# Kernel tuning notes

Measured on AMD Instinct MI355X. Metric: run time of the kernel, lower is better.

## Reference

```python
import jax, jax.numpy as jnp
import numpy as np

N_QUBITS = 10
Q_DEPTH = 6
MAX_LAYERS = 15
DIM = 2 ** N_QUBITS
INV_SQRT2 = 0.7071067811865476

# PennyLane ordering: wire 0 is the most-significant bit of the state index.
# All gates (H, RY, CNOT) are real, so the state stays real float32.

def _split(state, wire):
    a = 2 ** wire
    b = 2 ** (N_QUBITS - wire - 1)
    return state.reshape(-1, a, 2, b)

def apply_h(state, wire):
    s = _split(state, wire)
    s0, s1 = s[:, :, 0], s[:, :, 1]
    out = jnp.stack([(s0 + s1) * INV_SQRT2, (s0 - s1) * INV_SQRT2], axis=2)
    return out.reshape(-1, DIM)

def apply_ry(state, theta, wire):
    # theta: scalar (shared weight) or (B,) per-sample angle
    c = jnp.cos(theta * 0.5).reshape(-1, 1, 1)
    sn = jnp.sin(theta * 0.5).reshape(-1, 1, 1)
    s = _split(state, wire)
    s0, s1 = s[:, :, 0], s[:, :, 1]
    out = jnp.stack([c * s0 - sn * s1, sn * s0 + c * s1], axis=2)
    return out.reshape(-1, DIM)

def apply_cnot(state, ctrl):
    # CNOT on adjacent wires [ctrl, ctrl+1]
    a = 2 ** ctrl
    b = 2 ** (N_QUBITS - ctrl - 2)
    s = state.reshape(-1, a, 2, 2, b)
    out = jnp.stack([s[:, :, 0], s[:, :, 1, ::-1]], axis=2)
    return out.reshape(-1, DIM)

def expval_z(state):
    # <Z_j> = P(qubit j = 0) - P(qubit j = 1)
    zs = []
    for w in range(N_QUBITS):
        s = _split(state, w)
        p = s * s
        zs.append(jnp.sum(p[:, :, 0], axis=(1, 2)) - jnp.sum(p[:, :, 1], axis=(1, 2)))
    return jnp.stack(zs, axis=1)  # (B, n_qubits)

def simulate(q_in, q_params):
    B = q_in.shape[0]
    qw = q_params.reshape(MAX_LAYERS, N_QUBITS)
    state = jnp.zeros((B, DIM), q_in.dtype).at[:, 0].set(1.0)
    for w in range(N_QUBITS):
        state = apply_h(state, w)
    for w in range(N_QUBITS):
        state = apply_ry(state, q_in[:, w], w)
    for k in range(Q_DEPTH):
        for i in range(0, N_QUBITS - 1, 2):
            state = apply_cnot(state, i)
        for i in range(1, N_QUBITS - 1, 2):
            state = apply_cnot(state, i)
        for w in range(N_QUBITS):
            state = apply_ry(state, qw[k + 1, w], w)
    return expval_z(state)

def setup_inputs() -> dict:
    key = jax.random.key(0)
    k1, k2, k3, k4, k5 = jax.random.split(key, 5)
    B, D_IN, N_CLASSES = 8192, 512, 2
    return {
        "input_features": jax.random.normal(k1, (B, D_IN), jnp.float32),
        "W_red": jax.random.normal(k2, (N_QUBITS, D_IN), jnp.float32) * 0.04,
        "b_red": jnp.zeros((N_QUBITS,), jnp.float32),
        "q_params": 0.01 * jax.random.normal(k3, (MAX_LAYERS * N_QUBITS,), jnp.float32),
        "W_post": jax.random.normal(k4, (N_CLASSES, N_QUBITS), jnp.float32) * 0.3,
        "b_post": jax.random.normal(k5, (N_CLASSES,), jnp.float32) * 0.01,
    }

def reference(input_features, W_red, b_red, q_params, W_post, b_post):
    pre_out = input_features @ W_red.T + b_red           # (B, n_qubits)
    q_in = jnp.tanh(pre_out) * (np.pi / 2.0)             # angles in (-pi/2, pi/2)
    q_out = simulate(q_in, q_params)                     # (B, n_qubits) PauliZ expvals
    return q_out @ W_post.T + b_post                     # (B, n_classes)
```

## Files before the change

### kernel.cpp

```cpp
#include <hip/hip_runtime.h>
#include <math.h>

#define QDEPTH 6


__device__ __forceinline__ float shx(float v, int m) { return __shfl_xor(v, m, 64); }

template<int CTRL>
__device__ __forceinline__ float dpp_mov(float v) {
  int i = __float_as_int(v);
  int r = __builtin_amdgcn_update_dpp(i, i, CTRL, 0xF, 0xF, true);
  return __int_as_float(r);
}

template<int CTRL>
__device__ __forceinline__ float dpp_add0(float v) {
  int i = __float_as_int(v);
  int r = __builtin_amdgcn_update_dpp(0, i, CTRL, 0xF, 0xF, false);
  return v + __int_as_float(r);
}

__device__ __forceinline__ float wave_sum(float v) {
  v = dpp_add0<0x111>(v);
  v = dpp_add0<0x112>(v);
  v = dpp_add0<0x114>(v);
  v = dpp_add0<0x118>(v);
  v = dpp_add0<0x142>(v);
  v = dpp_add0<0x143>(v);
  return v;
}

__device__ __forceinline__ float bcast63(float v) {
  return __int_as_float(__builtin_amdgcn_readlane(__float_as_int(v), 63));
}

__device__ __forceinline__ void pl32_swap(float& a, float& b) {
  asm("v_permlane32_swap_b32 %0, %1" : "+v"(a), "+v"(b));
}
__device__ __forceinline__ void pl16_swap(float& a, float& b) {
  asm("v_permlane16_swap_b32 %0, %1" : "+v"(a), "+v"(b));
}

template<bool IS32>
__device__ __forceinline__ void ry_pl(float (&x)[16], float c, float s) {
#pragma unroll
  for (int r = 0; r < 16; r += 2) {
    float a = x[r], b = x[r + 1];
    if (IS32) pl32_swap(a, b); else pl16_swap(a, b);
    float n0 = c * a - s * b;
    float n1 = s * a + c * b;
    if (IS32) pl32_swap(n0, n1); else pl16_swap(n0, n1);
    x[r] = n0; x[r + 1] = n1;
  }
}

template<int CTRL>
__device__ __forceinline__ void ry_dpp(float (&x)[16], float c, float sg) {
#pragma unroll
  for (int r = 0; r < 16; ++r) {
    float p = dpp_mov<CTRL>(x[r]);
    x[r] = c * x[r] + sg * p;
  }
}

template<int M>
__device__ __forceinline__ void ry_sh(float (&x)[16], float c, float sg) {
#pragma unroll
  for (int r = 0; r < 16; ++r) {
    float p = shx(x[r], M);
    x[r] = c * x[r] + sg * p;
  }
}

template<int JM>
__device__ __forceinline__ void ry_reg(float (&x)[16], float c, float s) {
#pragma unroll
  for (int r = 0; r < 16; ++r)
    if (!(r & JM)) {
      float x0 = x[r], x1 = x[r | JM];
      x[r]      = c * x0 - s * x1;
      x[r | JM] = s * x0 + c * x1;
    }
}

template<int MC, int MT>
__device__ __forceinline__ void cnot_rr(float (&x)[16]) {
#pragma unroll
  for (int r = 0; r < 16; ++r)
    if ((r & MC) && !(r & MT)) {
      float t = x[r]; x[r] = x[r | MT]; x[r | MT] = t;
    }
}

__device__ __forceinline__ void cnot_lr56(float (&x)[16], int lane) {
  bool cb = lane & 1;
#pragma unroll
  for (int r = 0; r < 8; ++r) {
    float lo = x[r], hi = x[r + 8];
    x[r]     = cb ? hi : lo;
    x[r + 8] = cb ? lo : hi;
  }
}

__global__ void __launch_bounds__(256) qnet_kernel(
    const float* __restrict__ inp,
    const float* __restrict__ Wred,
    const float* __restrict__ bred,
    const float* __restrict__ qp,
    const float* __restrict__ Wpost,
    const float* __restrict__ bpost,
    float* __restrict__ out,
    int B) {
  int tid  = blockIdx.x * 256 + threadIdx.x;
  int wv   = tid >> 6;
  int lane = tid & 63;
  if (wv >= B) return;

  int o = lane ^ (((lane >> 4) & 1) << 3) ^ (((lane >> 2) & 1) << 1);
  int psrc = o ^ (((o >> 5) & 1) << 4) ^ (((o >> 3) & 1) << 2) ^ ((o >> 1) & 1);

  const float4* row4 = (const float4*)(inp + (size_t)wv * 512);
  float4 a0 = row4[lane], a1 = row4[lane + 64];
  float th[10];
#pragma unroll
  for (int q = 0; q < 10; ++q) {
    const float4* w4 = (const float4*)(Wred + q * 512);
    float4 b0 = w4[lane], b1 = w4[lane + 64];
    float t = a0.x * b0.x + a0.y * b0.y + a0.z * b0.z + a0.w * b0.w;
    t += a1.x * b1.x + a1.y * b1.y + a1.z * b1.z + a1.w * b1.w;
    th[q] = t;
  }

  float g0[10], g1[10];
#pragma unroll
  for (int q = 0; q < 10; ++q) {
    float tot = bcast63(wave_sum(th[q])) + bred[q];
    float xc = fminf(fmaxf(tot, -15.f), 15.f);
    float u = __expf(2.f * xc);
    float tanhv = (u - 1.f) * __builtin_amdgcn_rcpf(u + 1.f);
    float t = tanhv * 0.78539816339744831f;
    float c = __cosf(t), s = __sinf(t);
    g0[q] = (c - s) * 0.70710678118654752f;
    g1[q] = (c + s) * 0.70710678118654752f;
  }
  float lf = 1.f;
#pragma unroll
  for (int w = 0; w < 6; ++w)
    lf *= ((lane >> (5 - w)) & 1) ? g1[w] : g0[w];
  float f67[4], f89[4];
#pragma unroll
  for (int i = 0; i < 4; ++i) {
    f67[i] = ((i & 2) ? g1[6] : g0[6]) * ((i & 1) ? g1[7] : g0[7]);
    f89[i] = ((i & 2) ? g1[8] : g0[8]) * ((i & 1) ? g1[9] : g0[9]);
  }
  float x[16];
#pragma unroll
  for (int r = 0; r < 16; ++r) x[r] = lf * f67[r >> 2] * f89[r & 3];

#pragma unroll
  for (int k = 0; k < QDEPTH; ++k) {
    const float* qr = qp + (k + 1) * 10;
#pragma unroll
    for (int r = 0; r < 16; ++r) x[r] = __shfl(x[r], psrc, 64);
    cnot_rr<8, 4>(x);
    cnot_rr<2, 1>(x);
    cnot_lr56(x, lane);
    cnot_rr<4, 2>(x);

    float t, c, s, sg;
    t = qr[0] * 0.5f; c = __cosf(t); s = __sinf(t); ry_pl<true>(x, c, s);
    t = qr[1] * 0.5f; c = __cosf(t); s = __sinf(t); ry_pl<false>(x, c, s);
    t = qr[2] * 0.5f; c = __cosf(t); s = __sinf(t);
    sg = (lane & 8) ? s : -s; ry_sh<8>(x, c, sg);
    t = qr[3] * 0.5f; c = __cosf(t); s = __sinf(t);
    sg = (lane & 4) ? s : -s; ry_sh<4>(x, c, sg);
    t = qr[4] * 0.5f; c = __cosf(t); s = __sinf(t);
    sg = (lane & 2) ? s : -s; ry_dpp<0x4E>(x, c, sg);
    t = qr[5] * 0.5f; c = __cosf(t); s = __sinf(t);
    sg = (lane & 1) ? s : -s; ry_dpp<0xB1>(x, c, sg);
    t = qr[6] * 0.5f; c = __cosf(t); s = __sinf(t); ry_reg<8>(x, c, s);
    t = qr[7] * 0.5f; c = __cosf(t); s = __sinf(t); ry_reg<4>(x, c, s);
    t = qr[8] * 0.5f; c = __cosf(t); s = __sinf(t); ry_reg<2>(x, c, s);
    t = qr[9] * 0.5f; c = __cosf(t); s = __sinf(t); ry_reg<1>(x, c, s);
  }

  float S = 0.f, z6 = 0.f, z7 = 0.f, z8 = 0.f, z9 = 0.f;
#pragma unroll
  for (int r = 0; r < 16; ++r) {
    float q2 = x[r] * x[r];
    S  += q2;
    z6 += (r & 8) ? -q2 : q2;
    z7 += (r & 4) ? -q2 : q2;
    z8 += (r & 2) ? -q2 : q2;
    z9 += (r & 1) ? -q2 : q2;
  }
  float A0 = 0.f, A1 = 0.f;
#pragma unroll
  for (int w = 0; w < 6; ++w) {
    bool b = (lane >> (5 - w)) & 1;
    A0 += b ? -Wpost[w] : Wpost[w];
    A1 += b ? -Wpost[10 + w] : Wpost[10 + w];
  }
  float o0 = A0 * S + Wpost[6] * z6 + Wpost[7] * z7 + Wpost[8] * z8 + Wpost[9] * z9;
  float o1 = A1 * S + Wpost[16] * z6 + Wpost[17] * z7 + Wpost[18] * z8 + Wpost[19] * z9;
  o0 = wave_sum(o0);
  o1 = wave_sum(o1);
  if (lane == 63) {
    out[2 * (size_t)wv]     = o0 + bpost[0];
    out[2 * (size_t)wv + 1] = o1 + bpost[1];
  }
}

extern "C" void kernel_launch(void* const* d_in, const int* in_sizes, int n_in,
                              void* d_out, int out_size, void* d_ws, size_t ws_size,
                              hipStream_t stream) {
  const float* inp   = (const float*)d_in[0];
  const float* Wred  = (const float*)d_in[1];
  const float* bred  = (const float*)d_in[2];
  const float* qp    = (const float*)d_in[3];
  const float* Wpost = (const float*)d_in[4];
  const float* bpost = (const float*)d_in[5];
  float* out = (float*)d_out;

  int B = in_sizes[0] / 512;
  int threads = 256;
  int blocks = (B * 64 + threads - 1) / threads;
  qnet_kernel<<<blocks, threads, 0, stream>>>(inp, Wred, bred, qp, Wpost, bpost, out, B);
}
```

Measured before the change: 113.3 us.

## Pack state amplitudes into float2 pairs and use packed FP32 math

Reorganizes the 16 per-lane amplitudes into 8 float2 pairs and applies the RY gates with v_pk_fma/v_pk_mul packed FP32 instructions, halving the VALU instruction count for the rotation arithmetic. The CNOT permutations and the in-register RY gates are reordered and remapped so that the lane-bit CNOT becomes a per-lane coefficient selection inside the qubit-6 rotation, and the qubit-9 pair rotation is folded into the swap pattern. Inline asm for the packed ops may block compiler scheduling and fusion, and the shuffles and DPP moves still run per scalar, so the gains depend on how much of the time is arithmetic versus cross-lane movement.

New measurement: 109.8 us. 1.03x faster.

```diff
diff --git a/kernel.cpp b/kernel.cpp
--- a/kernel.cpp
+++ b/kernel.cpp
@@ -2,6 +2,8 @@
 #include <math.h>
 
 #define QDEPTH 6
+
+typedef float f2 __attribute__((ext_vector_type(2)));
 
 
 __device__ __forceinline__ float shx(float v, int m) { return __shfl_xor(v, m, 64); }
@@ -41,65 +43,11 @@
   asm("v_permlane16_swap_b32 %0, %1" : "+v"(a), "+v"(b));
 }
 
-template<bool IS32>
-__device__ __forceinline__ void ry_pl(float (&x)[16], float c, float s) {
-#pragma unroll
-  for (int r = 0; r < 16; r += 2) {
-    float a = x[r], b = x[r + 1];
-    if (IS32) pl32_swap(a, b); else pl16_swap(a, b);
-    float n0 = c * a - s * b;
-    float n1 = s * a + c * b;
-    if (IS32) pl32_swap(n0, n1); else pl16_swap(n0, n1);
-    x[r] = n0; x[r + 1] = n1;
-  }
-}
-
-template<int CTRL>
-__device__ __forceinline__ void ry_dpp(float (&x)[16], float c, float sg) {
-#pragma unroll
-  for (int r = 0; r < 16; ++r) {
-    float p = dpp_mov<CTRL>(x[r]);
-    x[r] = c * x[r] + sg * p;
-  }
-}
-
-template<int M>
-__device__ __forceinline__ void ry_sh(float (&x)[16], float c, float sg) {
-#pragma unroll
-  for (int r = 0; r < 16; ++r) {
-    float p = shx(x[r], M);
-    x[r] = c * x[r] + sg * p;
-  }
-}
-
-template<int JM>
-__device__ __forceinline__ void ry_reg(float (&x)[16], float c, float s) {
-#pragma unroll
-  for (int r = 0; r < 16; ++r)
-    if (!(r & JM)) {
-      float x0 = x[r], x1 = x[r | JM];
-      x[r]      = c * x0 - s * x1;
-      x[r | JM] = s * x0 + c * x1;
-    }
-}
-
-template<int MC, int MT>
-__device__ __forceinline__ void cnot_rr(float (&x)[16]) {
-#pragma unroll
-  for (int r = 0; r < 16; ++r)
-    if ((r & MC) && !(r & MT)) {
-      float t = x[r]; x[r] = x[r | MT]; x[r | MT] = t;
-    }
-}
-
-__device__ __forceinline__ void cnot_lr56(float (&x)[16], int lane) {
-  bool cb = lane & 1;
-#pragma unroll
-  for (int r = 0; r < 8; ++r) {
-    float lo = x[r], hi = x[r + 8];
-    x[r]     = cb ? hi : lo;
-    x[r + 8] = cb ? lo : hi;
-  }
+__device__ __forceinline__ f2 pk_mul(f2 a, f2 b) {
+  f2 d; asm("v_pk_mul_f32 %0, %1, %2" : "=v"(d) : "v"(a), "v"(b)); return d;
+}
+__device__ __forceinline__ f2 pk_fma(f2 a, f2 b, f2 c) {
+  f2 d; asm("v_pk_fma_f32 %0, %1, %2, %3" : "=v"(d) : "v"(a), "v"(b), "v"(c)); return d;
 }
 
 __global__ void __launch_bounds__(256) qnet_kernel(
@@ -147,53 +95,158 @@
 #pragma unroll
   for (int w = 0; w < 6; ++w)
     lf *= ((lane >> (5 - w)) & 1) ? g1[w] : g0[w];
-  float f67[4], f89[4];
-#pragma unroll
-  for (int i = 0; i < 4; ++i) {
-    f67[i] = ((i & 2) ? g1[6] : g0[6]) * ((i & 1) ? g1[7] : g0[7]);
-    f89[i] = ((i & 2) ? g1[8] : g0[8]) * ((i & 1) ? g1[9] : g0[9]);
-  }
-  float x[16];
-#pragma unroll
-  for (int r = 0; r < 16; ++r) x[r] = lf * f67[r >> 2] * f89[r & 3];
+  float f67v[4];
+#pragma unroll
+  for (int j = 0; j < 4; ++j)
+    f67v[j] = ((j & 2) ? g1[6] : g0[6]) * ((j & 1) ? g1[7] : g0[7]);
+  f2 F89v[2];
+  F89v[0] = (f2){ g0[8] * g0[9], g0[8] * g1[9] };
+  F89v[1] = (f2){ g1[8] * g0[9], g1[8] * g1[9] };
+  f2 x2[8];
+#pragma unroll
+  for (int i = 0; i < 8; ++i) {
+    float m = lf * f67v[i >> 1];
+    x2[i] = (f2){ m * F89v[i & 1].x, m * F89v[i & 1].y };
+  }
+
+  bool cb = lane & 1;
 
 #pragma unroll
   for (int k = 0; k < QDEPTH; ++k) {
     const float* qr = qp + (k + 1) * 10;
-#pragma unroll
-    for (int r = 0; r < 16; ++r) x[r] = __shfl(x[r], psrc, 64);
-    cnot_rr<8, 4>(x);
-    cnot_rr<2, 1>(x);
-    cnot_lr56(x, lane);
-    cnot_rr<4, 2>(x);
-
-    float t, c, s, sg;
-    t = qr[0] * 0.5f; c = __cosf(t); s = __sinf(t); ry_pl<true>(x, c, s);
-    t = qr[1] * 0.5f; c = __cosf(t); s = __sinf(t); ry_pl<false>(x, c, s);
-    t = qr[2] * 0.5f; c = __cosf(t); s = __sinf(t);
-    sg = (lane & 8) ? s : -s; ry_sh<8>(x, c, sg);
-    t = qr[3] * 0.5f; c = __cosf(t); s = __sinf(t);
-    sg = (lane & 4) ? s : -s; ry_sh<4>(x, c, sg);
-    t = qr[4] * 0.5f; c = __cosf(t); s = __sinf(t);
-    sg = (lane & 2) ? s : -s; ry_dpp<0x4E>(x, c, sg);
-    t = qr[5] * 0.5f; c = __cosf(t); s = __sinf(t);
-    sg = (lane & 1) ? s : -s; ry_dpp<0xB1>(x, c, sg);
-    t = qr[6] * 0.5f; c = __cosf(t); s = __sinf(t); ry_reg<8>(x, c, s);
-    t = qr[7] * 0.5f; c = __cosf(t); s = __sinf(t); ry_reg<4>(x, c, s);
-    t = qr[8] * 0.5f; c = __cosf(t); s = __sinf(t); ry_reg<2>(x, c, s);
-    t = qr[9] * 0.5f; c = __cosf(t); s = __sinf(t); ry_reg<1>(x, c, s);
-  }
-
-  float S = 0.f, z6 = 0.f, z7 = 0.f, z8 = 0.f, z9 = 0.f;
-#pragma unroll
-  for (int r = 0; r < 16; ++r) {
-    float q2 = x[r] * x[r];
-    S  += q2;
-    z6 += (r & 8) ? -q2 : q2;
-    z7 += (r & 4) ? -q2 : q2;
-    z8 += (r & 2) ? -q2 : q2;
-    z9 += (r & 1) ? -q2 : q2;
-  }
+
+#pragma unroll
+    for (int i = 0; i < 8; ++i) {
+      float lo = __shfl(x2[i].x, psrc, 64);
+      float hi = __shfl(x2[i].y, psrc, 64);
+      x2[i] = (f2){lo, hi};
+    }
+    { f2 t = x2[4]; x2[4] = x2[6]; x2[6] = t;
+      t = x2[5]; x2[5] = x2[7]; x2[7] = t; }
+    { f2 t = x2[2]; x2[2] = x2[3]; x2[3] = t;
+      t = x2[6]; x2[6] = x2[7]; x2[7] = t; }
+
+    { float t9 = qr[9] * 0.5f; float c = __cosf(t9), s = __sinf(t9);
+#pragma unroll
+      for (int i = 0; i < 8; ++i) {
+        bool flg = (i == 1 || i == 2 || i == 5 || i == 6);
+        float lo = x2[i].x, hi = x2[i].y;
+        float nlo, nhi;
+        if (flg) { nlo = c * hi - s * lo; nhi = s * hi + c * lo; }
+        else     { nlo = c * lo - s * hi; nhi = s * lo + c * hi; }
+        x2[i] = (f2){nlo, nhi};
+      } }
+
+    { float t6 = qr[6] * 0.5f; float c = __cosf(t6), s = __sinf(t6);
+      float Ac = cb ? -s : c;  float Bc = cb ? c : -s;
+      float Cc = cb ? c : s;   float Dc = cb ? s : c;
+      f2 AA = {Ac, Ac}, BB = {Bc, Bc}, CC = {Cc, Cc}, DD = {Dc, Dc};
+#pragma unroll
+      for (int i = 0; i < 4; ++i) {
+        f2 u = x2[i], w = x2[i + 4];
+        x2[i]     = pk_fma(u, AA, pk_mul(w, BB));
+        x2[i + 4] = pk_fma(u, CC, pk_mul(w, DD));
+      } }
+
+    { float t7 = qr[7] * 0.5f; float c = __cosf(t7), s = __sinf(t7);
+      f2 cc = {c, c}, ss = {s, s}, ns = {-s, -s};
+#pragma unroll
+      for (int i = 0; i < 8; ++i) if (!(i & 2)) {
+        f2 u = x2[i], w = x2[i | 2];
+        x2[i]     = pk_fma(u, cc, pk_mul(w, ns));
+        x2[i | 2] = pk_fma(w, cc, pk_mul(u, ss));
+      } }
+
+    { float t8 = qr[8] * 0.5f; float c = __cosf(t8), s = __sinf(t8);
+      f2 cc = {c, c}, ss = {s, s}, ns = {-s, -s};
+#pragma unroll
+      for (int i = 0; i < 8; ++i) if (!(i & 1)) {
+        f2 u = x2[i], w = x2[i | 1];
+        x2[i]     = pk_fma(u, cc, pk_mul(w, ns));
+        x2[i | 1] = pk_fma(w, cc, pk_mul(u, ss));
+      } }
+
+    { float t0 = qr[0] * 0.5f; float c = __cosf(t0), s = __sinf(t0);
+      f2 cc = {c, c}, ss = {s, s}, ns = {-s, -s};
+#pragma unroll
+      for (int j = 0; j < 4; ++j) {
+        float ax = x2[2 * j].x,     ay = x2[2 * j].y;
+        float bx = x2[2 * j + 1].x, by = x2[2 * j + 1].y;
+        pl32_swap(ax, bx); pl32_swap(ay, by);
+        f2 u = {ax, ay}, v = {bx, by};
+        f2 nu = pk_fma(u, cc, pk_mul(v, ns));
+        f2 nv = pk_fma(v, cc, pk_mul(u, ss));
+        float nux = nu.x, nuy = nu.y, nvx = nv.x, nvy = nv.y;
+        pl32_swap(nux, nvx); pl32_swap(nuy, nvy);
+        x2[2 * j] = (f2){nux, nuy}; x2[2 * j + 1] = (f2){nvx, nvy};
+      } }
+
+    { float t1 = qr[1] * 0.5f; float c = __cosf(t1), s = __sinf(t1);
+      f2 cc = {c, c}, ss = {s, s}, ns = {-s, -s};
+#pragma unroll
+      for (int j = 0; j < 4; ++j) {
+        float ax = x2[2 * j].x,     ay = x2[2 * j].y;
+        float bx = x2[2 * j + 1].x, by = x2[2 * j + 1].y;
+        pl16_swap(ax, bx); pl16_swap(ay, by);
+        f2 u = {ax, ay}, v = {bx, by};
+        f2 nu = pk_fma(u, cc, pk_mul(v, ns));
+        f2 nv = pk_fma(v, cc, pk_mul(u, ss));
+        float nux = nu.x, nuy = nu.y, nvx = nv.x, nvy = nv.y;
+        pl16_swap(nux, nvx); pl16_swap(nuy, nvy);
+        x2[2 * j] = (f2){nux, nuy}; x2[2 * j + 1] = (f2){nvx, nvy};
+      } }
+
+    { float t2 = qr[2] * 0.5f; float c = __cosf(t2), s = __sinf(t2);
+      float sg = (lane & 8) ? s : -s;
+      f2 cc = {c, c}, gg = {sg, sg};
+#pragma unroll
+      for (int i = 0; i < 8; ++i) {
+        f2 p = { shx(x2[i].x, 8), shx(x2[i].y, 8) };
+        x2[i] = pk_fma(x2[i], cc, pk_mul(p, gg));
+      } }
+
+    { float t3 = qr[3] * 0.5f; float c = __cosf(t3), s = __sinf(t3);
+      float sg = (lane & 4) ? s : -s;
+      f2 cc = {c, c}, gg = {sg, sg};
+#pragma unroll
+      for (int i = 0; i < 8; ++i) {
+        f2 p = { shx(x2[i].x, 4), shx(x2[i].y, 4) };
+        x2[i] = pk_fma(x2[i], cc, pk_mul(p, gg));
+      } }
+
+    { float t4 = qr[4] * 0.5f; float c = __cosf(t4), s = __sinf(t4);
+      float sg = (lane & 2) ? s : -s;
+      f2 cc = {c, c}, gg = {sg, sg};
+#pragma unroll
+      for (int i = 0; i < 8; ++i) {
+        f2 p = { dpp_mov<0x4E>(x2[i].x), dpp_mov<0x4E>(x2[i].y) };
+        x2[i] = pk_fma(x2[i], cc, pk_mul(p, gg));
+      } }
+
+    { float t5 = qr[5] * 0.5f; float c = __cosf(t5), s = __sinf(t5);
+      float sg = (lane & 1) ? s : -s;
+      f2 cc = {c, c}, gg = {sg, sg};
+#pragma unroll
+      for (int i = 0; i < 8; ++i) {
+        f2 p = { dpp_mov<0xB1>(x2[i].x), dpp_mov<0xB1>(x2[i].y) };
+        x2[i] = pk_fma(x2[i], cc, pk_mul(p, gg));
+      } }
+  }
+
+  f2 one = {1.f, 1.f}, mone = {-1.f, -1.f};
+  f2 P = {0.f, 0.f}, P6 = {0.f, 0.f}, P7 = {0.f, 0.f}, P8 = {0.f, 0.f};
+#pragma unroll
+  for (int i = 0; i < 8; ++i) {
+    f2 sq = pk_mul(x2[i], x2[i]);
+    P  = pk_fma(sq, one, P);
+    P6 = pk_fma(sq, (i & 4) ? mone : one, P6);
+    P7 = pk_fma(sq, (i & 2) ? mone : one, P7);
+    P8 = pk_fma(sq, (i & 1) ? mone : one, P8);
+  }
+  float S  = P.x + P.y;
+  float z9 = P.x - P.y;
+  float z6 = P6.x + P6.y, z7 = P7.x + P7.y, z8 = P8.x + P8.y;
+
   float A0 = 0.f, A1 = 0.f;
 #pragma unroll
   for (int w = 0; w < 6; ++w) {
```

## Simulate statevector in packed fp16 with precomputed gate coefficients

Applied to the files above, without the earlier changes.

Stores the per-wave 1024-amplitude state as 8 packed half2 registers instead of 16 floats, so gates run on packed fp16 math and each lane shuffle moves two amplitudes at once. A separate setup kernel precomputes the RY cos/sin coefficients as half2 pairs in workspace, which removes per-wave trig. It also remaps the qubit-to-register layout so wire 9 pairs within a half2 and is handled by a half-swap. The risk is lost accuracy from fp16 over 60 rotations, plus an extra kernel launch.

Measured after the change: 99.25 us. 12.4% less time.

```diff
diff --git a/kernel.cpp b/kernel.cpp
--- a/kernel.cpp
+++ b/kernel.cpp
@@ -3,14 +3,29 @@
 
 #define QDEPTH 6
 
-
-__device__ __forceinline__ float shx(float v, int m) { return __shfl_xor(v, m, 64); }
+typedef _Float16 h2 __attribute__((ext_vector_type(2)));
+
+__device__ __forceinline__ int   h2i(h2 v)  { return __builtin_bit_cast(int, v); }
+__device__ __forceinline__ h2    ih2(int v) { return __builtin_bit_cast(h2, v); }
+
+__device__ __forceinline__ h2 hswap(h2 v) {
+  unsigned u = __builtin_bit_cast(unsigned, v);
+  u = (u >> 16) | (u << 16);
+  return __builtin_bit_cast(h2, u);
+}
+
+__device__ __forceinline__ h2 cvt_pk(float a, float b) {
+  return __builtin_bit_cast(h2, __builtin_amdgcn_cvt_pkrtz(a, b));
+}
+
+__device__ __forceinline__ h2 bper(int addr, h2 v) {
+  return ih2(__builtin_amdgcn_ds_bpermute(addr, h2i(v)));
+}
 
 template<int CTRL>
-__device__ __forceinline__ float dpp_mov(float v) {
-  int i = __float_as_int(v);
-  int r = __builtin_amdgcn_update_dpp(i, i, CTRL, 0xF, 0xF, true);
-  return __int_as_float(r);
+__device__ __forceinline__ h2 dpph(h2 v) {
+  int i = h2i(v);
+  return ih2(__builtin_amdgcn_update_dpp(i, i, CTRL, 0xF, 0xF, true));
 }
 
 template<int CTRL>
@@ -34,71 +49,31 @@
   return __int_as_float(__builtin_amdgcn_readlane(__float_as_int(v), 63));
 }
 
-__device__ __forceinline__ void pl32_swap(float& a, float& b) {
+__device__ __forceinline__ void pl32s(int& a, int& b) {
   asm("v_permlane32_swap_b32 %0, %1" : "+v"(a), "+v"(b));
 }
-__device__ __forceinline__ void pl16_swap(float& a, float& b) {
+__device__ __forceinline__ void pl16s(int& a, int& b) {
   asm("v_permlane16_swap_b32 %0, %1" : "+v"(a), "+v"(b));
 }
 
-template<bool IS32>
-__device__ __forceinline__ void ry_pl(float (&x)[16], float c, float s) {
-#pragma unroll
-  for (int r = 0; r < 16; r += 2) {
-    float a = x[r], b = x[r + 1];
-    if (IS32) pl32_swap(a, b); else pl16_swap(a, b);
-    float n0 = c * a - s * b;
-    float n1 = s * a + c * b;
-    if (IS32) pl32_swap(n0, n1); else pl16_swap(n0, n1);
-    x[r] = n0; x[r + 1] = n1;
-  }
-}
-
-template<int CTRL>
-__device__ __forceinline__ void ry_dpp(float (&x)[16], float c, float sg) {
-#pragma unroll
-  for (int r = 0; r < 16; ++r) {
-    float p = dpp_mov<CTRL>(x[r]);
-    x[r] = c * x[r] + sg * p;
-  }
-}
-
-template<int M>
-__device__ __forceinline__ void ry_sh(float (&x)[16], float c, float sg) {
-#pragma unroll
-  for (int r = 0; r < 16; ++r) {
-    float p = shx(x[r], M);
-    x[r] = c * x[r] + sg * p;
-  }
-}
-
-template<int JM>
-__device__ __forceinline__ void ry_reg(float (&x)[16], float c, float s) {
-#pragma unroll
-  for (int r = 0; r < 16; ++r)
-    if (!(r & JM)) {
-      float x0 = x[r], x1 = x[r | JM];
-      x[r]      = c * x0 - s * x1;
-      x[r | JM] = s * x0 + c * x1;
-    }
-}
-
-template<int MC, int MT>
-__device__ __forceinline__ void cnot_rr(float (&x)[16]) {
-#pragma unroll
-  for (int r = 0; r < 16; ++r)
-    if ((r & MC) && !(r & MT)) {
-      float t = x[r]; x[r] = x[r | MT]; x[r | MT] = t;
-    }
-}
-
-__device__ __forceinline__ void cnot_lr56(float (&x)[16], int lane) {
-  bool cb = lane & 1;
-#pragma unroll
-  for (int r = 0; r < 8; ++r) {
-    float lo = x[r], hi = x[r + 8];
-    x[r]     = cb ? hi : lo;
-    x[r + 8] = cb ? lo : hi;
+__global__ void setup_kernel(const float* __restrict__ qp, unsigned* __restrict__ cb) {
+  int t = threadIdx.x;
+  if (t >= 60) return;
+  int k = t / 10, w = t % 10;
+  float ang = qp[(k + 1) * 10 + w] * 0.5f;
+  float c = __cosf(ang), s = __sinf(ang);
+  unsigned* p = cb + k * 32 + ((w < 9) ? w * 3 : 27);
+  h2 cc = { (_Float16)c, (_Float16)c };
+  if (w < 9) {
+    h2 ss = { (_Float16)s,  (_Float16)s };
+    h2 ns = { (_Float16)(-s), (_Float16)(-s) };
+    p[0] = __builtin_bit_cast(unsigned, cc);
+    p[1] = __builtin_bit_cast(unsigned, ss);
+    p[2] = __builtin_bit_cast(unsigned, ns);
+  } else {
+    h2 ms = { (_Float16)(-s), (_Float16)s };
+    p[0] = __builtin_bit_cast(unsigned, cc);
+    p[1] = __builtin_bit_cast(unsigned, ms);
   }
 }
 
@@ -106,7 +81,7 @@
     const float* __restrict__ inp,
     const float* __restrict__ Wred,
     const float* __restrict__ bred,
-    const float* __restrict__ qp,
+    const unsigned* __restrict__ cb,
     const float* __restrict__ Wpost,
     const float* __restrict__ bpost,
     float* __restrict__ out,
@@ -118,6 +93,10 @@
 
   int o = lane ^ (((lane >> 4) & 1) << 3) ^ (((lane >> 2) & 1) << 1);
   int psrc = o ^ (((o >> 5) & 1) << 4) ^ (((o >> 3) & 1) << 2) ^ ((o >> 1) & 1);
+  int addrP  = psrc << 2;
+  int addrX8 = (lane ^ 8) << 2;
+  int addrX4 = (lane ^ 4) << 2;
+  bool cb1 = lane & 1;
 
   const float4* row4 = (const float4*)(inp + (size_t)wv * 512);
   float4 a0 = row4[lane], a1 = row4[lane + 64];
@@ -147,53 +126,143 @@
 #pragma unroll
   for (int w = 0; w < 6; ++w)
     lf *= ((lane >> (5 - w)) & 1) ? g1[w] : g0[w];
-  float f67[4], f89[4];
-#pragma unroll
-  for (int i = 0; i < 4; ++i) {
-    f67[i] = ((i & 2) ? g1[6] : g0[6]) * ((i & 1) ? g1[7] : g0[7]);
-    f89[i] = ((i & 2) ? g1[8] : g0[8]) * ((i & 1) ? g1[9] : g0[9]);
-  }
-  float x[16];
-#pragma unroll
-  for (int r = 0; r < 16; ++r) x[r] = lf * f67[r >> 2] * f89[r & 3];
-
-#pragma unroll
+  float f67v[4];
+#pragma unroll
+  for (int j = 0; j < 4; ++j)
+    f67v[j] = ((j & 2) ? g1[6] : g0[6]) * ((j & 1) ? g1[7] : g0[7]);
+  float F89x[2], F89y[2];
+  F89x[0] = g0[8] * g0[9]; F89y[0] = g0[8] * g1[9];
+  F89x[1] = g1[8] * g0[9]; F89y[1] = g1[8] * g1[9];
+
+  h2 x[8];
+#pragma unroll
+  for (int i = 0; i < 8; ++i) {
+    float m = lf * f67v[i >> 1];
+    x[i] = cvt_pk(m * F89x[i & 1], m * F89y[i & 1]);
+  }
+
   for (int k = 0; k < QDEPTH; ++k) {
-    const float* qr = qp + (k + 1) * 10;
-#pragma unroll
-    for (int r = 0; r < 16; ++r) x[r] = __shfl(x[r], psrc, 64);
-    cnot_rr<8, 4>(x);
-    cnot_rr<2, 1>(x);
-    cnot_lr56(x, lane);
-    cnot_rr<4, 2>(x);
-
-    float t, c, s, sg;
-    t = qr[0] * 0.5f; c = __cosf(t); s = __sinf(t); ry_pl<true>(x, c, s);
-    t = qr[1] * 0.5f; c = __cosf(t); s = __sinf(t); ry_pl<false>(x, c, s);
-    t = qr[2] * 0.5f; c = __cosf(t); s = __sinf(t);
-    sg = (lane & 8) ? s : -s; ry_sh<8>(x, c, sg);
-    t = qr[3] * 0.5f; c = __cosf(t); s = __sinf(t);
-    sg = (lane & 4) ? s : -s; ry_sh<4>(x, c, sg);
-    t = qr[4] * 0.5f; c = __cosf(t); s = __sinf(t);
-    sg = (lane & 2) ? s : -s; ry_dpp<0x4E>(x, c, sg);
-    t = qr[5] * 0.5f; c = __cosf(t); s = __sinf(t);
-    sg = (lane & 1) ? s : -s; ry_dpp<0xB1>(x, c, sg);
-    t = qr[6] * 0.5f; c = __cosf(t); s = __sinf(t); ry_reg<8>(x, c, s);
-    t = qr[7] * 0.5f; c = __cosf(t); s = __sinf(t); ry_reg<4>(x, c, s);
-    t = qr[8] * 0.5f; c = __cosf(t); s = __sinf(t); ry_reg<2>(x, c, s);
-    t = qr[9] * 0.5f; c = __cosf(t); s = __sinf(t); ry_reg<1>(x, c, s);
-  }
-
-  float S = 0.f, z6 = 0.f, z7 = 0.f, z8 = 0.f, z9 = 0.f;
-#pragma unroll
-  for (int r = 0; r < 16; ++r) {
-    float q2 = x[r] * x[r];
-    S  += q2;
-    z6 += (r & 8) ? -q2 : q2;
-    z7 += (r & 4) ? -q2 : q2;
-    z8 += (r & 2) ? -q2 : q2;
-    z9 += (r & 1) ? -q2 : q2;
-  }
+    const unsigned* L = cb + k * 32;
+    h2 cc9 = ih2(L[27]), ms9 = ih2(L[28]);
+    h2 cc6 = ih2(L[18]), ss6 = ih2(L[19]), ns6 = ih2(L[20]);
+    h2 cc7 = ih2(L[21]), ss7 = ih2(L[22]), ns7 = ih2(L[23]);
+    h2 cc8 = ih2(L[24]), ss8 = ih2(L[25]), ns8 = ih2(L[26]);
+    h2 cc0 = ih2(L[0]),  ss0 = ih2(L[1]),  ns0 = ih2(L[2]);
+    h2 cc1 = ih2(L[3]),  ss1 = ih2(L[4]),  ns1 = ih2(L[5]);
+    h2 cc2 = ih2(L[6]),  ss2 = ih2(L[7]),  ns2 = ih2(L[8]);
+    h2 cc3 = ih2(L[9]),  ss3 = ih2(L[10]), ns3 = ih2(L[11]);
+    h2 cc4 = ih2(L[12]), ss4 = ih2(L[13]), ns4 = ih2(L[14]);
+    h2 cc5 = ih2(L[15]), ss5 = ih2(L[16]), ns5 = ih2(L[17]);
+
+#pragma unroll
+    for (int i = 0; i < 8; ++i) x[i] = bper(addrP, x[i]);
+    { h2 t = x[4]; x[4] = x[6]; x[6] = t; t = x[5]; x[5] = x[7]; x[7] = t; }
+    { h2 t = x[2]; x[2] = x[3]; x[3] = t; t = x[6]; x[6] = x[7]; x[7] = t; }
+
+#pragma unroll
+    for (int i = 0; i < 8; ++i) {
+      h2 t = hswap(x[i]);
+      bool flg = (i == 1 || i == 2 || i == 5 || i == 6);
+      x[i] = flg ? (h2)(t * cc9 + x[i] * ms9) : (h2)(x[i] * cc9 + t * ms9);
+    }
+
+    {
+      h2 AA = cb1 ? ns6 : cc6;
+      h2 BB = cb1 ? cc6 : ns6;
+      h2 CC = cb1 ? cc6 : ss6;
+      h2 DD = cb1 ? ss6 : cc6;
+#pragma unroll
+      for (int i = 0; i < 4; ++i) {
+        h2 u = x[i], w = x[i + 4];
+        x[i]     = u * AA + w * BB;
+        x[i + 4] = u * CC + w * DD;
+      }
+    }
+#pragma unroll
+    for (int i = 0; i < 8; ++i) if (!(i & 2)) {
+      h2 u = x[i], w = x[i | 2];
+      x[i]     = u * cc7 + w * ns7;
+      x[i | 2] = w * cc7 + u * ss7;
+    }
+#pragma unroll
+    for (int i = 0; i < 8; ++i) if (!(i & 1)) {
+      h2 u = x[i], w = x[i | 1];
+      x[i]     = u * cc8 + w * ns8;
+      x[i | 1] = w * cc8 + u * ss8;
+    }
+
+#pragma unroll
+    for (int j = 0; j < 4; ++j) {
+      int a = h2i(x[2 * j]), b = h2i(x[2 * j + 1]);
+      pl32s(a, b);
+      h2 u = ih2(a), v = ih2(b);
+      h2 nu = u * cc0 + v * ns0;
+      h2 nv = v * cc0 + u * ss0;
+      int na = h2i(nu), nb = h2i(nv);
+      pl32s(na, nb);
+      x[2 * j] = ih2(na); x[2 * j + 1] = ih2(nb);
+    }
+#pragma unroll
+    for (int j = 0; j < 4; ++j) {
+      int a = h2i(x[2 * j]), b = h2i(x[2 * j + 1]);
+      pl16s(a, b);
+      h2 u = ih2(a), v = ih2(b);
+      h2 nu = u * cc1 + v * ns1;
+      h2 nv = v * cc1 + u * ss1;
+      int na = h2i(nu), nb = h2i(nv);
+      pl16s(na, nb);
+      x[2 * j] = ih2(na); x[2 * j + 1] = ih2(nb);
+    }
+    {
+      h2 gg = (lane & 8) ? ss2 : ns2;
+#pragma unroll
+      for (int i = 0; i < 8; ++i) {
+        h2 p = bper(addrX8, x[i]);
+        x[i] = x[i] * cc2 + p * gg;
+      }
+    }
+    {
+      h2 gg = (lane & 4) ? ss3 : ns3;
+#pragma unroll
+      for (int i = 0; i < 8; ++i) {
+        h2 p = bper(addrX4, x[i]);
+        x[i] = x[i] * cc3 + p * gg;
+      }
+    }
+    {
+      h2 gg = (lane & 2) ? ss4 : ns4;
+#pragma unroll
+      for (int i = 0; i < 8; ++i) {
+        h2 p = dpph<0x4E>(x[i]);
+        x[i] = x[i] * cc4 + p * gg;
+      }
+    }
+    {
+      h2 gg = (lane & 1) ? ss5 : ns5;
+#pragma unroll
+      for (int i = 0; i < 8; ++i) {
+        h2 p = dpph<0xB1>(x[i]);
+        x[i] = x[i] * cc5 + p * gg;
+      }
+    }
+  }
+
+  float q[8], d9 = 0.f;
+#pragma unroll
+  for (int i = 0; i < 8; ++i) {
+    float lo = (float)x[i].x, hi = (float)x[i].y;
+    float a2 = lo * lo, b2 = hi * hi;
+    q[i] = a2 + b2;
+    d9 += a2 - b2;
+  }
+  float A = q[0] + q[1], Bq = q[2] + q[3], C = q[4] + q[5], D = q[6] + q[7];
+  float S  = (A + Bq) + (C + D);
+  float z6 = (A + Bq) - (C + D);
+  float z7 = (A - Bq) + (C - D);
+  float E = q[0] - q[1], F = q[2] - q[3], G = q[4] - q[5], H = q[6] - q[7];
+  float z8 = (E + F) + (G + H);
+  float z9 = d9;
+
   float A0 = 0.f, A1 = 0.f;
 #pragma unroll
   for (int w = 0; w < 6; ++w) {
@@ -221,9 +290,11 @@
   const float* Wpost = (const float*)d_in[4];
   const float* bpost = (const float*)d_in[5];
   float* out = (float*)d_out;
+  unsigned* cbuf = (unsigned*)d_ws;
 
   int B = in_sizes[0] / 512;
+  setup_kernel<<<1, 64, 0, stream>>>(qp, cbuf);
   int threads = 256;
   int blocks = (B * 64 + threads - 1) / threads;
-  qnet_kernel<<<blocks, threads, 0, stream>>>(inp, Wred, bred, qp, Wpost, bpost, out, B);
-}
+  qnet_kernel<<<blocks, threads, 0, stream>>>(inp, Wred, bred, cbuf, Wpost, bpost, out, B);
+}
```
